# Kernel tuning notes

Measured on AMD Instinct MI355X. Metric: run time of the kernel, lower is better.

The kernel has to match this reference:

```python
import jax, jax.numpy as jnp
import numpy as np

EPS = 1e-12  # matches torch F.normalize eps
TEMPERATURE = 1.0
LAMBDA = 0.8


def _l2norm(x):
    n = jnp.sqrt(jnp.sum(x * x, axis=-1, keepdims=True))
    return x / jnp.maximum(n, EPS)


def setup_inputs() -> dict:
    key = jax.random.key(0)
    feats = jax.random.normal(key, (4, 4096, 512), dtype=jnp.float32)
    return {"feats": feats, "node": 8}


def reference(feats, node):
    f = _l2norm(feats)                                   # [B,N,D]
    scores = jnp.einsum('bnd,bmd->bnm', f, f) / TEMPERATURE  # [B,N,N]
    vals, idx = jax.lax.top_k(scores, node)              # [B,N,k]
    B, N, _ = scores.shape
    bi = jnp.arange(B)[:, None, None]
    ni = jnp.arange(N)[None, :, None]
    sparse = jnp.full_like(scores, -jnp.inf).at[bi, ni, idx].set(vals)
    w = jax.nn.softmax(sparse, axis=-1)                  # zeros outside top-k
    feats_att = jnp.einsum('bnm,bmd->bnd', w, f)
    feats_gam = f * LAMBDA + feats_att * (1.0 - LAMBDA)
    return _l2norm(feats_gam)
```

## Files before the change

### kernel.cpp

```cpp
#include <hip/hip_runtime.h>
#include <stdint.h>

#define NROWS 4096
#define NDIM  512
#define NTILE 32
#define NPAIR 528
#define TOPT  8
#define NLIST 32
#define NCAND 256
#define NRESC 12
#define KSEL  8

typedef __attribute__((ext_vector_type(8))) short short8;
typedef __attribute__((ext_vector_type(4))) float f32x4;

__device__ __forceinline__ unsigned short f2bf(float x) {
  unsigned int u = __float_as_uint(x);
  return (unsigned short)((u + 0x7fffu + ((u >> 16) & 1u)) >> 16);
}

__device__ __forceinline__ void gl_lds16(const void* g, void* l) {
  void* gnc = (void*)g;
  __builtin_amdgcn_global_load_lds(
      (__attribute__((address_space(1))) void*)gnc,
      (__attribute__((address_space(3))) void*)l, 16, 0, 0);
}

__device__ __forceinline__ void ins8(unsigned int (&tv)[TOPT], unsigned int k) {
#pragma unroll
  for (int j = 0; j < TOPT; ++j) {
    const unsigned int nt = tv[j] > k ? tv[j] : k;
    k = tv[j] > k ? k : tv[j];
    tv[j] = nt;
  }
}

__device__ __forceinline__ void ce_desc(unsigned int& x, unsigned int& y) {
  const unsigned int hi = x > y ? x : y, lo = x > y ? y : x;
  x = hi; y = lo;
}
__device__ __forceinline__ void bitonic8_desc(unsigned int (&a)[TOPT]) {
  ce_desc(a[0], a[4]); ce_desc(a[1], a[5]); ce_desc(a[2], a[6]); ce_desc(a[3], a[7]);
  ce_desc(a[0], a[2]); ce_desc(a[1], a[3]); ce_desc(a[4], a[6]); ce_desc(a[5], a[7]);
  ce_desc(a[0], a[1]); ce_desc(a[2], a[3]); ce_desc(a[4], a[5]); ce_desc(a[6], a[7]);
}
__device__ __forceinline__ void xormerge(unsigned int (&a)[TOPT], int xm) {
  unsigned int ov[TOPT];
#pragma unroll
  for (int j = 0; j < TOPT; ++j) ov[j] = __shfl_xor(a[j], xm, 64);
  unsigned int r[TOPT];
#pragma unroll
  for (int j = 0; j < TOPT; ++j) r[j] = a[j] > ov[TOPT - 1 - j] ? a[j] : ov[TOPT - 1 - j];
#pragma unroll
  for (int j = 0; j < TOPT; ++j) a[j] = r[j];
}

__global__ __launch_bounds__(256) void k_norm(const float* __restrict__ in,
                                              unsigned short* __restrict__ fbf,
                                              float* __restrict__ invn) {
  const int row = blockIdx.x * 4 + (threadIdx.x >> 6);
  const int l = threadIdx.x & 63;
  const float4* src = reinterpret_cast<const float4*>(in + (size_t)row * NDIM);
  float4 a = src[l * 2], b = src[l * 2 + 1];
  float ss = a.x * a.x + a.y * a.y + a.z * a.z + a.w * a.w +
             b.x * b.x + b.y * b.y + b.z * b.z + b.w * b.w;
#pragma unroll
  for (int off = 32; off; off >>= 1) ss += __shfl_xor(ss, off, 64);
  const float inv = 1.0f / fmaxf(sqrtf(ss), 1e-12f);
  if (l == 0) invn[row] = inv;
  a.x *= inv; a.y *= inv; a.z *= inv; a.w *= inv;
  b.x *= inv; b.y *= inv; b.z *= inv; b.w *= inv;
  uint4 ub;
  ub.x = (unsigned)f2bf(a.x) | ((unsigned)f2bf(a.y) << 16);
  ub.y = (unsigned)f2bf(a.z) | ((unsigned)f2bf(a.w) << 16);
  ub.z = (unsigned)f2bf(b.x) | ((unsigned)f2bf(b.y) << 16);
  ub.w = (unsigned)f2bf(b.z) | ((unsigned)f2bf(b.w) << 16);
  reinterpret_cast<uint4*>(fbf + (size_t)row * NDIM)[l] = ub;
}

__global__ __launch_bounds__(512, 4) void k_coarse(const unsigned short* __restrict__ fbf,
                                                   unsigned int* __restrict__ keys) {
  __shared__ alignas(16) struct {
    union {
      struct { unsigned short A[128 * 64]; unsigned short B[128 * 64]; } st;
      unsigned short S[128 * 128];
    } u;
    unsigned short T[128 * 128];
  } sh;

  const int tid = threadIdx.x;
  const int w = tid >> 6, l = tid & 63;

  const int lin = blockIdx.x;
  const int zb = lin / NPAIR;
  int rem = lin - zb * NPAIR;
  int ti = 0;
  while (rem >= NTILE - ti) { rem -= NTILE - ti; ++ti; }
  const int tj = ti + rem;

  const int q0 = ti * 128;
  const int m0 = tj * 128;
  const int bbase = zb * NROWS;
  const bool diag = (ti == tj);

  const int qh = w >> 2, mq = w & 3;
  const int r = tid >> 2, sub = tid & 3;
  const int rx = r & 31;

  const int lrow = (l >> 3);
  const int lkg  = ((l & 7) ^ lrow) * 8;

  const f32x4 vzero = {0.f, 0.f, 0.f, 0.f};
  f32x4 acc[4][2];
#pragma unroll
  for (int i = 0; i < 4; ++i)
#pragma unroll
    for (int j = 0; j < 2; ++j) acc[i][j] = vzero;

  for (int kt = 0; kt < 8; ++kt) {
    const int kk = kt * 64;
#pragma unroll
    for (int t = 0; t < 2; ++t) {
      const int sa = w * 2 + t;
      const int srow = sa * 8 + lrow;
      gl_lds16(fbf + ((size_t)(bbase + q0 + srow) << 9) + kk + lkg,
               &sh.u.st.A[sa * 512]);
      if (!diag)
        gl_lds16(fbf + ((size_t)(bbase + m0 + srow) << 9) + kk + lkg,
                 &sh.u.st.B[sa * 512]);
    }
    __syncthreads();
    const unsigned short* Bb = diag ? sh.u.st.A : sh.u.st.B;
#pragma unroll
    for (int ks = 0; ks < 2; ++ks) {
      short8 av[4], bv[2];
      const int kgrp = ks * 4 + (l >> 4);
#pragma unroll
      for (int i = 0; i < 4; ++i) {
        const int row = qh * 64 + i * 16 + (l & 15);
        av[i] = *(const short8*)&sh.u.st.A[row * 64 + (kgrp ^ (l & 7)) * 8];
      }
#pragma unroll
      for (int j = 0; j < 2; ++j) {
        const int row = mq * 32 + j * 16 + (l & 15);
        bv[j] = *(const short8*)&Bb[row * 64 + (kgrp ^ (l & 7)) * 8];
      }
#pragma unroll
      for (int i = 0; i < 4; ++i)
#pragma unroll
        for (int j = 0; j < 2; ++j)
          acc[i][j] = __builtin_amdgcn_mfma_f32_16x16x32_bf16(av[i], bv[j], acc[i][j], 0, 0, 0);
    }
    __syncthreads();
  }

#pragma unroll
  for (int i = 0; i < 4; ++i) {
    const int qb_ = qh * 64 + i * 16 + (l >> 4) * 4;
#pragma unroll
    for (int j = 0; j < 2; ++j) {
      const int mc = mq * 32 + j * 16 + (l & 15);
#pragma unroll
      for (int rr = 0; rr < 4; ++rr) {
        const int q = qb_ + rr;
        unsigned int uu = __float_as_uint(acc[i][j][rr]);
        uu ^= (unsigned int)(((int)uu) >> 31) | 0x80000000u;
        const unsigned short k16 = (unsigned short)(uu >> 16);
        const int pg = ((mc >> 2) ^ (q & 31));
        sh.u.S[q * 128 + pg * 4 + (mc & 3)] = k16;
        const int pgt = ((q >> 2) ^ (mc & 31));
        sh.T[mc * 128 + pgt * 4 + (q & 3)] = k16;
      }
    }
  }
  __syncthreads();

  {
    unsigned int tv[TOPT];
#pragma unroll
    for (int j = 0; j < TOPT; ++j) tv[j] = 0u;
    const int invb0 = 4095 - (m0 + sub * 32);
#pragma unroll
    for (int cg = 0; cg < 8; ++cg) {
      const int pg = (sub * 8 + cg) ^ rx;
      const ushort4 s4 = *(const ushort4*)&sh.u.S[r * 128 + pg * 4];
      const unsigned int invb = (unsigned int)(invb0 - cg * 4);
      const unsigned int k0 = ((unsigned int)s4.x << 16) | invb;
      const unsigned int k1 = ((unsigned int)s4.y << 16) | (invb - 1);
      const unsigned int k2 = ((unsigned int)s4.z << 16) | (invb - 2);
      const unsigned int k3 = ((unsigned int)s4.w << 16) | (invb - 3);
      if (k0 > tv[TOPT - 1]) ins8(tv, k0);
      if (k1 > tv[TOPT - 1]) ins8(tv, k1);
      if (k2 > tv[TOPT - 1]) ins8(tv, k2);
      if (k3 > tv[TOPT - 1]) ins8(tv, k3);
    }
    xormerge(tv, 1);
    bitonic8_desc(tv);
    xormerge(tv, 2);
    if (sub == 0) {
      unsigned int* dst = keys + (((size_t)(bbase + q0 + r)) * NLIST + tj) * TOPT;
      reinterpret_cast<uint4*>(dst)[0] = make_uint4(tv[0], tv[1], tv[2], tv[3]);
      reinterpret_cast<uint4*>(dst)[1] = make_uint4(tv[4], tv[5], tv[6], tv[7]);
    }
  }

  if (!diag) {
    unsigned int tv[TOPT];
#pragma unroll
    for (int j = 0; j < TOPT; ++j) tv[j] = 0u;
    const int invb0 = 4095 - (q0 + sub * 32);
#pragma unroll
    for (int cg = 0; cg < 8; ++cg) {
      const int pg = (sub * 8 + cg) ^ rx;
      const ushort4 s4 = *(const ushort4*)&sh.T[r * 128 + pg * 4];
      const unsigned int invb = (unsigned int)(invb0 - cg * 4);
      const unsigned int k0 = ((unsigned int)s4.x << 16) | invb;
      const unsigned int k1 = ((unsigned int)s4.y << 16) | (invb - 1);
      const unsigned int k2 = ((unsigned int)s4.z << 16) | (invb - 2);
      const unsigned int k3 = ((unsigned int)s4.w << 16) | (invb - 3);
      if (k0 > tv[TOPT - 1]) ins8(tv, k0);
      if (k1 > tv[TOPT - 1]) ins8(tv, k1);
      if (k2 > tv[TOPT - 1]) ins8(tv, k2);
      if (k3 > tv[TOPT - 1]) ins8(tv, k3);
    }
    xormerge(tv, 1);
    bitonic8_desc(tv);
    xormerge(tv, 2);
    if (sub == 0) {
      unsigned int* dst = keys + (((size_t)(bbase + m0 + r)) * NLIST + ti) * TOPT;
      reinterpret_cast<uint4*>(dst)[0] = make_uint4(tv[0], tv[1], tv[2], tv[3]);
      reinterpret_cast<uint4*>(dst)[1] = make_uint4(tv[4], tv[5], tv[6], tv[7]);
    }
  }
}

__global__ __launch_bounds__(256) void k_sel(const float* __restrict__ feats,
                                             const float* __restrict__ invn,
                                             const unsigned int* __restrict__ keys,
                                             uint2* __restrict__ selw) {
  __shared__ int sh_si[4][NRESC];

  const int lin = blockIdx.x;
  const int xcd = lin & 7;
  const int slot = lin >> 3;
  const int b = xcd >> 1;
  const int wv = threadIdx.x >> 6;
  const int n = ((xcd & 1) * 512 + slot) * 4 + wv;
  const int qg = b * NROWS + n;
  const int l = threadIdx.x & 63;

  const uint4 kv = reinterpret_cast<const uint4*>(keys + (size_t)qg * NCAND)[l];
  const unsigned int ka = kv.x, kb = kv.y, kc = kv.z, kd = kv.w;

  unsigned int T = 0u;
#pragma unroll
  for (int bit = 31; bit >= 0; --bit) {
    const unsigned int Tp = T | (1u << bit);
    const int cnt = (int)__popcll(__ballot(ka >= Tp)) +
                    (int)__popcll(__ballot(kb >= Tp)) +
                    (int)__popcll(__ballot(kc >= Tp)) +
                    (int)__popcll(__ballot(kd >= Tp));
    T = (cnt >= NRESC) ? Tp : T;
  }

  {
    const unsigned long long mA = __ballot(ka >= T);
    const unsigned long long mB = __ballot(kb >= T);
    const unsigned long long mC = __ballot(kc >= T);
    const unsigned long long mD = __ballot(kd >= T);
    const unsigned long long lt = (1ull << l) - 1ull;
    const int oB = (int)__popcll(mA);
    const int oC = oB + (int)__popcll(mB);
    const int oD = oC + (int)__popcll(mC);
    if (ka >= T) sh_si[wv][(int)__popcll(mA & lt)] = 4095 - (int)(ka & 4095u);
    if (kb >= T) sh_si[wv][oB + (int)__popcll(mB & lt)] = 4095 - (int)(kb & 4095u);
    if (kc >= T) sh_si[wv][oC + (int)__popcll(mC & lt)] = 4095 - (int)(kc & 4095u);
    if (kd >= T) sh_si[wv][oD + (int)__popcll(mD & lt)] = 4095 - (int)(kd & 4095u);
  }
  asm volatile("s_waitcnt lgkmcnt(0)" ::: "memory");
  __builtin_amdgcn_sched_barrier(0);

  int si[NRESC];
#pragma unroll
  for (int j = 0; j < NRESC; ++j)
    si[j] = __builtin_amdgcn_readfirstlane(sh_si[wv][j]);

  const float* __restrict__ fb = feats + (size_t)b * NROWS * NDIM;
  const float* frow = fb + (size_t)n * NDIM;
  const float ia = invn[qg];
  float selfv[8];
#pragma unroll
  for (int c = 0; c < 8; ++c) selfv[c] = frow[c * 64 + l] * ia;

  double ex[NRESC];
#pragma unroll
  for (int rr = 0; rr < NRESC; ++rr) {
    const float* g = fb + (size_t)si[rr] * NDIM;
    const float ib = invn[b * NROWS + si[rr]];
    double s = 0.0;
#pragma unroll
    for (int c = 0; c < 8; ++c)
      s += (double)selfv[c] * (double)(g[c * 64 + l] * ib);
    ex[rr] = s;
  }
#pragma unroll
  for (int off = 32; off; off >>= 1) {
#pragma unroll
    for (int rr = 0; rr < NRESC; ++rr) ex[rr] += __shfl_xor(ex[rr], off, 64);
  }

  unsigned mask = 0;
  double wex[KSEL]; int wi[KSEL];
#pragma unroll
  for (int rr = 0; rr < KSEL; ++rr) {
    double mv = -1.0e300; int midx = 0x7fffffff; int mslot = 0;
#pragma unroll
    for (int j = 0; j < NRESC; ++j) {
      const bool avail = ((mask >> j) & 1u) == 0u;
      if (avail && (ex[j] > mv || (ex[j] == mv && si[j] < midx))) {
        mv = ex[j]; midx = si[j]; mslot = j;
      }
    }
    mask |= 1u << mslot;
    wex[rr] = mv; wi[rr] = midx;
  }

  float w8[KSEL];
  const float mx = (float)wex[0];
  float wsum = 0.f;
#pragma unroll
  for (int rr = 0; rr < KSEL; ++rr) { w8[rr] = expf((float)wex[rr] - mx); wsum += w8[rr]; }
  const float cs = 0.2f / wsum;

  uint2 osel = make_uint2(0u, 0u);
#pragma unroll
  for (int rr = 0; rr < KSEL; ++rr) {
    if (l == rr) osel = make_uint2((unsigned)wi[rr], __float_as_uint(cs * w8[rr]));
  }
  if (l < KSEL) selw[(size_t)qg * KSEL + l] = osel;
}

__global__ __launch_bounds__(256) void k_blend(const float* __restrict__ feats,
                                               const float* __restrict__ invn,
                                               const uint2* __restrict__ selw,
                                               float* __restrict__ out) {
  const int row = blockIdx.x * 4 + (threadIdx.x >> 6);
  const int b = row >> 12;
  const int l = threadIdx.x & 63;

  const uint2* pw = selw + (size_t)row * KSEL;
  uint2 p[KSEL];
#pragma unroll
  for (int j = 0; j < KSEL; ++j) p[j] = pw[j];

  const float* __restrict__ fb = feats + (size_t)b * NROWS * NDIM;
  const float* frow = feats + (size_t)row * NDIM;
  const float ia = invn[row];

  float acc[8];
#pragma unroll
  for (int c = 0; c < 8; ++c) acc[c] = 0.8f * (frow[c * 64 + l] * ia);
#pragma unroll
  for (int j = 0; j < KSEL; ++j) {
    const float* g = fb + (size_t)p[j].x * NDIM;
    const float ib = invn[b * NROWS + (int)p[j].x];
    const float wr = __uint_as_float(p[j].y);
#pragma unroll
    for (int c = 0; c < 8; ++c) acc[c] = fmaf(wr, g[c * 64 + l] * ib, acc[c]);
  }

  float ss = 0.f;
#pragma unroll
  for (int c = 0; c < 8; ++c) ss += acc[c] * acc[c];
#pragma unroll
  for (int off = 32; off; off >>= 1) ss += __shfl_xor(ss, off, 64);
  const float inv = 1.0f / fmaxf(sqrtf(ss), 1e-12f);
  float* orow = out + (size_t)row * NDIM;
#pragma unroll
  for (int c = 0; c < 8; ++c) orow[c * 64 + l] = acc[c] * inv;
}

extern "C" void kernel_launch(void* const* d_in, const int* in_sizes, int n_in,
                              void* d_out, int out_size, void* d_ws, size_t ws_size,
                              hipStream_t stream) {
  (void)in_sizes; (void)n_in; (void)out_size; (void)ws_size;
  const float* feats = (const float*)d_in[0];
  char* ws = (char*)d_ws;
  unsigned short* fbf  = (unsigned short*)(ws);
  unsigned int*   keys = (unsigned int*)(ws + 16777216);
  float*          invn = (float*)(ws + 33554432);
  uint2*          selw = (uint2*)(ws + 33619968);
  float* out = (float*)d_out;

  k_norm  <<<dim3(4096), dim3(256), 0, stream>>>(feats, fbf, invn);
  k_coarse<<<dim3(4 * NPAIR), dim3(512), 0, stream>>>(fbf, keys);
  k_sel   <<<dim3(4096), dim3(256), 0, stream>>>(feats, invn, keys, selw);
  k_blend <<<dim3(4096), dim3(256), 0, stream>>>(feats, invn, selw, out);
}
```

Before: 246.7 us.

## Fuse rescoring/selection and blend kernels, reusing gathered neighbor rows in registers

Merges the selection kernel and the blend kernel into one. The 12 rescored candidate rows are loaded once into registers and reused for both the exact dot products and the weighted blend, so the second gather of 8 neighbor rows and the selw round trip go away. Sequential top-8 extraction is replaced by rank counting, with non-top-8 weights masked to zero. This saves one launch and roughly half the gather traffic, at the cost of higher register pressure (96 floats held per lane) and FMAs over 12 rows instead of 8.

Result: slower. 334.7 us (+35.7%).

```diff
diff --git a/kernel.cpp b/kernel.cpp
--- a/kernel.cpp
+++ b/kernel.cpp
@@ -234,10 +234,10 @@
   }
 }
 
-__global__ __launch_bounds__(256) void k_sel(const float* __restrict__ feats,
-                                             const float* __restrict__ invn,
-                                             const unsigned int* __restrict__ keys,
-                                             uint2* __restrict__ selw) {
+__global__ __launch_bounds__(256) void k_fuse(const float* __restrict__ feats,
+                                              const float* __restrict__ invn,
+                                              const unsigned int* __restrict__ keys,
+                                              float* __restrict__ out) {
   __shared__ int sh_si[4][NRESC];
 
   const int lin = blockIdx.x;
@@ -292,15 +292,21 @@
 #pragma unroll
   for (int c = 0; c < 8; ++c) selfv[c] = frow[c * 64 + l] * ia;
 
-  double ex[NRESC];
+  float gv[NRESC][8];
 #pragma unroll
   for (int rr = 0; rr < NRESC; ++rr) {
     const float* g = fb + (size_t)si[rr] * NDIM;
     const float ib = invn[b * NROWS + si[rr]];
+#pragma unroll
+    for (int c = 0; c < 8; ++c) gv[rr][c] = g[c * 64 + l] * ib;
+  }
+
+  double ex[NRESC];
+#pragma unroll
+  for (int rr = 0; rr < NRESC; ++rr) {
     double s = 0.0;
 #pragma unroll
-    for (int c = 0; c < 8; ++c)
-      s += (double)selfv[c] * (double)(g[c * 64 + l] * ib);
+    for (int c = 0; c < 8; ++c) s += (double)selfv[c] * (double)gv[rr][c];
     ex[rr] = s;
   }
 #pragma unroll
@@ -309,64 +315,42 @@
     for (int rr = 0; rr < NRESC; ++rr) ex[rr] += __shfl_xor(ex[rr], off, 64);
   }
 
-  unsigned mask = 0;
-  double wex[KSEL]; int wi[KSEL];
-#pragma unroll
-  for (int rr = 0; rr < KSEL; ++rr) {
-    double mv = -1.0e300; int midx = 0x7fffffff; int mslot = 0;
-#pragma unroll
-    for (int j = 0; j < NRESC; ++j) {
-      const bool avail = ((mask >> j) & 1u) == 0u;
-      if (avail && (ex[j] > mv || (ex[j] == mv && si[j] < midx))) {
-        mv = ex[j]; midx = si[j]; mslot = j;
+  int rank_[NRESC];
+#pragma unroll
+  for (int j = 0; j < NRESC; ++j) {
+    int rk = 0;
+#pragma unroll
+    for (int a = 0; a < NRESC; ++a) {
+      if (a != j) {
+        const bool beats = (ex[a] > ex[j]) || (ex[a] == ex[j] && si[a] < si[j]);
+        rk += beats ? 1 : 0;
       }
     }
-    mask |= 1u << mslot;
-    wex[rr] = mv; wi[rr] = midx;
-  }
-
-  float w8[KSEL];
-  const float mx = (float)wex[0];
+    rank_[j] = rk;
+  }
+  double mxd = ex[0];
+#pragma unroll
+  for (int j = 1; j < NRESC; ++j) mxd = ex[j] > mxd ? ex[j] : mxd;
+
+  const float mxf = (float)mxd;
+  float wj[NRESC];
   float wsum = 0.f;
 #pragma unroll
-  for (int rr = 0; rr < KSEL; ++rr) { w8[rr] = expf((float)wex[rr] - mx); wsum += w8[rr]; }
+  for (int j = 0; j < NRESC; ++j) {
+    const float e = expf((float)ex[j] - mxf);
+    wj[j] = (rank_[j] < KSEL) ? e : 0.f;
+    wsum += wj[j];
+  }
   const float cs = 0.2f / wsum;
 
-  uint2 osel = make_uint2(0u, 0u);
-#pragma unroll
-  for (int rr = 0; rr < KSEL; ++rr) {
-    if (l == rr) osel = make_uint2((unsigned)wi[rr], __float_as_uint(cs * w8[rr]));
-  }
-  if (l < KSEL) selw[(size_t)qg * KSEL + l] = osel;
-}
-
-__global__ __launch_bounds__(256) void k_blend(const float* __restrict__ feats,
-                                               const float* __restrict__ invn,
-                                               const uint2* __restrict__ selw,
-                                               float* __restrict__ out) {
-  const int row = blockIdx.x * 4 + (threadIdx.x >> 6);
-  const int b = row >> 12;
-  const int l = threadIdx.x & 63;
-
-  const uint2* pw = selw + (size_t)row * KSEL;
-  uint2 p[KSEL];
-#pragma unroll
-  for (int j = 0; j < KSEL; ++j) p[j] = pw[j];
-
-  const float* __restrict__ fb = feats + (size_t)b * NROWS * NDIM;
-  const float* frow = feats + (size_t)row * NDIM;
-  const float ia = invn[row];
-
   float acc[8];
 #pragma unroll
-  for (int c = 0; c < 8; ++c) acc[c] = 0.8f * (frow[c * 64 + l] * ia);
-#pragma unroll
-  for (int j = 0; j < KSEL; ++j) {
-    const float* g = fb + (size_t)p[j].x * NDIM;
-    const float ib = invn[b * NROWS + (int)p[j].x];
-    const float wr = __uint_as_float(p[j].y);
-#pragma unroll
-    for (int c = 0; c < 8; ++c) acc[c] = fmaf(wr, g[c * 64 + l] * ib, acc[c]);
+  for (int c = 0; c < 8; ++c) acc[c] = 0.8f * selfv[c];
+#pragma unroll
+  for (int rr = 0; rr < NRESC; ++rr) {
+    const float wr = cs * wj[rr];
+#pragma unroll
+    for (int c = 0; c < 8; ++c) acc[c] = fmaf(wr, gv[rr][c], acc[c]);
   }
 
   float ss = 0.f;
@@ -375,7 +359,7 @@
 #pragma unroll
   for (int off = 32; off; off >>= 1) ss += __shfl_xor(ss, off, 64);
   const float inv = 1.0f / fmaxf(sqrtf(ss), 1e-12f);
-  float* orow = out + (size_t)row * NDIM;
+  float* orow = out + (size_t)qg * NDIM;
 #pragma unroll
   for (int c = 0; c < 8; ++c) orow[c * 64 + l] = acc[c] * inv;
 }
@@ -389,11 +373,9 @@
   unsigned short* fbf  = (unsigned short*)(ws);
   unsigned int*   keys = (unsigned int*)(ws + 16777216);
   float*          invn = (float*)(ws + 33554432);
-  uint2*          selw = (uint2*)(ws + 33619968);
   float* out = (float*)d_out;
 
   k_norm  <<<dim3(4096), dim3(256), 0, stream>>>(feats, fbf, invn);
   k_coarse<<<dim3(4 * NPAIR), dim3(512), 0, stream>>>(fbf, keys);
-  k_sel   <<<dim3(4096), dim3(256), 0, stream>>>(feats, invn, keys, selw);
-  k_blend <<<dim3(4096), dim3(256), 0, stream>>>(feats, invn, selw, out);
-}
+  k_fuse  <<<dim3(4096), dim3(256), 0, stream>>>(feats, invn, keys, out);
+}
```
